# Optimization experiments

Measured on AMD Instinct MI355X. Metric: run time of the kernel, lower is better.

## Reference

```python
import jax, jax.numpy as jnp
import numpy as np

DIM = 2048
NUM_HEADS = 4  # hardcoded in RetNext.__init__
HEAD_DIM = DIM // NUM_HEADS
B, T = 4, 4096


def setup_inputs() -> dict:
    key = jax.random.key(0)
    ks = jax.random.split(key, 7)
    s = 1.0 / np.sqrt(DIM)  # roughly nn.Linear init scale
    return {
        "x": jax.random.normal(ks[0], (B, T, DIM), dtype=jnp.float32),
        "Wk": jax.random.normal(ks[1], (DIM, DIM), dtype=jnp.float32) * s,
        "bk": jax.random.normal(ks[2], (DIM,), dtype=jnp.float32) * s,
        "Wq": jax.random.normal(ks[3], (DIM, DIM), dtype=jnp.float32) * s,
        "bq": jax.random.normal(ks[4], (DIM,), dtype=jnp.float32) * s,
        "Wv": jax.random.normal(ks[5], (DIM, DIM), dtype=jnp.float32) * s,
        "bv": jax.random.normal(ks[6], (DIM,), dtype=jnp.float32) * s,
    }


def reference(x, Wk, bk, Wq, bq, Wv, bv):
    bsz, seq_len, _ = x.shape
    # nn.Linear: y = x @ W.T + b
    k = x @ Wk.T + bk
    q = x @ Wq.T + bq
    v = x @ Wv.T + bv
    # (b, s, h, d) -> (b, h, s, d)
    k = k.reshape(bsz, seq_len, NUM_HEADS, HEAD_DIM).transpose(0, 2, 1, 3)
    q = q.reshape(bsz, seq_len, NUM_HEADS, HEAD_DIM).transpose(0, 2, 1, 3)
    v = v.reshape(bsz, seq_len, NUM_HEADS, HEAD_DIM).transpose(0, 2, 1, 3)
    # states = k^T @ v : (b, h, d, d)
    states = jnp.einsum("bhsd,bhse->bhde", k, v)
    # out = q @ states : (b, h, s, d) -- returned WITHOUT reshape, as in the source
    out = jnp.einsum("bhsd,bhde->bhse", q, states)
    return out
```

## Files before the change

### kernel.cpp

```cpp
#include <hip/hip_runtime.h>
#include <cstdint>
#include <cstddef>

typedef __bf16 bf16;
typedef bf16 bf16x8 __attribute__((ext_vector_type(8)));
typedef float f32x4 __attribute__((ext_vector_type(4)));
typedef unsigned short u16;
typedef u16 u16x4 __attribute__((ext_vector_type(4)));
typedef u16 u16x8 __attribute__((ext_vector_type(8)));

__device__ __forceinline__ u16 f2bf(float f) {
    uint32_t u = __builtin_bit_cast(uint32_t, f);
    u += 0x7FFFu + ((u >> 16) & 1u);
    return (u16)(u >> 16);
}

#define AS1C(p) ((const __attribute__((address_space(1))) uint32_t*)(p))
#define AS3(p)  ((__attribute__((address_space(3))) uint32_t*)(p))
#define MFMA16  __builtin_amdgcn_mfma_f32_16x16x32_bf16

__device__ __forceinline__ void gemm_core(const bf16* __restrict__ Ablk,
                                          const bf16* __restrict__ Btblk,
                                          int lda, int ldb, int K,
                                          f32x4 acc[4][4])
{
    __shared__ bf16 lA[4096];
    __shared__ bf16 lB[4096];

    const int tid  = threadIdx.x;
    const int wave = tid >> 6;
    const int lane = tid & 63;
    const int lrow = lane >> 2;
    const int kcol = (lane & 3) << 3;

    const bf16* ga0 = Ablk  + (size_t)(wave * 32 + lrow) * lda + kcol;
    const bf16* ga1 = ga0 + (size_t)16 * lda;
    const bf16* gb0 = Btblk + (size_t)(wave * 32 + lrow) * ldb + kcol;
    const bf16* gb1 = gb0 + (size_t)16 * ldb;
    bf16* la0 = &lA[wave * 1024];
    bf16* la1 = &lA[wave * 1024 + 512];
    bf16* lb0 = &lB[wave * 1024];
    bf16* lb1 = &lB[wave * 1024 + 512];

    const int wm    = (wave >> 1) * 64;
    const int wn    = (wave & 1) * 64;
    const int col16 = lane & 15;
    const int quad  = lane >> 4;
    const bf16* pa = &lA[(wm + col16) * 32 + quad * 8];
    const bf16* pb = &lB[(wn + col16) * 32 + quad * 8];

    for (int kb = 0; kb < K; kb += 32) {
        __builtin_amdgcn_global_load_lds(AS1C(ga0 + kb), AS3(la0), 16, 0, 0);
        __builtin_amdgcn_global_load_lds(AS1C(ga1 + kb), AS3(la1), 16, 0, 0);
        __builtin_amdgcn_global_load_lds(AS1C(gb0 + kb), AS3(lb0), 16, 0, 0);
        __builtin_amdgcn_global_load_lds(AS1C(gb1 + kb), AS3(lb1), 16, 0, 0);
        __syncthreads();

        bf16x8 av[4], bv[4];
        #pragma unroll
        for (int i = 0; i < 4; ++i) av[i] = *(const bf16x8*)(pa + i * 512);
        #pragma unroll
        for (int i = 0; i < 4; ++i) bv[i] = *(const bf16x8*)(pb + i * 512);

        #pragma unroll
        for (int mi = 0; mi < 4; ++mi)
            #pragma unroll
            for (int ni = 0; ni < 4; ++ni)
                acc[mi][ni] = MFMA16(av[mi], bv[ni], acc[mi][ni], 0, 0, 0);
        __syncthreads();
    }
}

__global__ __launch_bounds__(256) void cast_bf16(const float* __restrict__ src,
                                                 u16* __restrict__ dst, int n8)
{
    int i = blockIdx.x * 256 + threadIdx.x;
    if (i >= n8) return;
    const float4* s = (const float4*)src + (size_t)i * 2;
    float4 f0 = s[0], f1 = s[1];
    u16x8 o;
    o[0] = f2bf(f0.x); o[1] = f2bf(f0.y); o[2] = f2bf(f0.z); o[3] = f2bf(f0.w);
    o[4] = f2bf(f1.x); o[5] = f2bf(f1.y); o[6] = f2bf(f1.z); o[7] = f2bf(f1.w);
    *((u16x8*)dst + i) = o;
}

__global__ __launch_bounds__(512, 2) void gemm_qkv(
    const bf16* __restrict__ xb,
    const bf16* __restrict__ Wkb, const bf16* __restrict__ Wqb, const bf16* __restrict__ Wvb,
    const float* __restrict__ bk, const float* __restrict__ bq, const float* __restrict__ bv,
    u16* __restrict__ qout, u16* __restrict__ kT, u16* __restrict__ vT)
{
    __shared__ bf16 smem[49152];
    char* sm = (char*)smem;

    const int bx = blockIdx.x;
    const int by = blockIdx.y;
    const int region = by >> 3;
    const int nloc = (by & 7) << 8;

    const bf16* W     = (region == 0) ? Wkb : (region == 1) ? Wqb : Wvb;
    const float* bias = (region == 0) ? bk  : (region == 1) ? bq  : bv;

    const bf16* Ablk = xb + (size_t)bx * 256 * 2048;
    const bf16* Bblk = W  + (size_t)nloc * 2048;
    const int lda = 2048, ldb = 2048;
    const int NT = 2048 / 32;

    const int tid  = threadIdx.x;
    const int wave = tid >> 6;
    const int lane = tid & 63;
    const int col16 = lane & 15;
    const int quad  = lane >> 4;
    const int wm = (wave >> 2) * 128;
    const int wn = (wave & 3) * 64;

    const int P0 = tid * 16;
    const int T0 = P0 ^ ((P0 >> 2) & 0x70) ^ ((P0 >> 4) & 0x10);
    const int r0 = T0 >> 6;
    const int ce = (T0 & 63) >> 1;
    const bf16* gA0 = Ablk + (size_t)r0 * lda + ce;
    const bf16* gA1 = Ablk + (size_t)(r0 + 128) * lda + ce;
    const bf16* gB0 = Bblk + (size_t)r0 * ldb + ce;
    const bf16* gB1 = Bblk + (size_t)(r0 + 128) * ldb + ce;
    const int dA0 = wave * 1024;
    const int dA1 = 8192  + wave * 1024;
    const int dB0 = 16384 + wave * 1024;
    const int dB1 = 24576 + wave * 1024;

    int offA[8], offB[4];
    #pragma unroll
    for (int mi = 0; mi < 8; ++mi) {
        int T = (wm + mi * 16 + col16) * 64 + quad * 16;
        offA[mi] = T ^ ((T >> 2) & 0x70);
    }
    #pragma unroll
    for (int ni = 0; ni < 4; ++ni) {
        int T = (wn + ni * 16 + col16) * 64 + quad * 16;
        offB[ni] = 16384 + (T ^ ((T >> 2) & 0x70));
    }

    f32x4 acc[8][4] = {};

#define GLD(src, dst) __builtin_amdgcn_global_load_lds(AS1C(src), AS3(sm + (dst)), 16, 0, 0)

    GLD(gA0,      0 + dA0); GLD(gB0,      0 + dB0);
    GLD(gA1,      0 + dA1); GLD(gB1,      0 + dB1);
    GLD(gA0 + 32, 32768 + dA0); GLD(gB0 + 32, 32768 + dB0);
    GLD(gA1 + 32, 32768 + dA1); GLD(gB1 + 32, 32768 + dB1);
    asm volatile("s_waitcnt vmcnt(4)" ::: "memory");
    __builtin_amdgcn_s_barrier();
    asm volatile("" ::: "memory");

    int buf = 0, sb = 2;
    for (int t = 0; t < NT; ++t) {
        const int  bb  = buf * 32768;
        const int  sbb = sb  * 32768;
        const int  kb  = (t + 2) * 32;
        const bool st  = (t + 2) < NT;

        bf16x8 a0 = *(const bf16x8*)(sm + bb + offA[0]);
        bf16x8 a1 = *(const bf16x8*)(sm + bb + offA[1]);
        bf16x8 a2 = *(const bf16x8*)(sm + bb + offA[2]);
        bf16x8 a3 = *(const bf16x8*)(sm + bb + offA[3]);
        bf16x8 b0 = *(const bf16x8*)(sm + bb + offB[0]);
        bf16x8 b1 = *(const bf16x8*)(sm + bb + offB[1]);
        bf16x8 b2 = *(const bf16x8*)(sm + bb + offB[2]);
        bf16x8 b3 = *(const bf16x8*)(sm + bb + offB[3]);
        if (st) { GLD(gA0 + kb, sbb + dA0); GLD(gB0 + kb, sbb + dB0); }
        __builtin_amdgcn_s_setprio(1);
        acc[0][0] = MFMA16(a0, b0, acc[0][0], 0, 0, 0);
        acc[0][1] = MFMA16(a0, b1, acc[0][1], 0, 0, 0);
        acc[0][2] = MFMA16(a0, b2, acc[0][2], 0, 0, 0);
        acc[0][3] = MFMA16(a0, b3, acc[0][3], 0, 0, 0);
        acc[1][0] = MFMA16(a1, b0, acc[1][0], 0, 0, 0);
        acc[1][1] = MFMA16(a1, b1, acc[1][1], 0, 0, 0);
        acc[1][2] = MFMA16(a1, b2, acc[1][2], 0, 0, 0);
        acc[1][3] = MFMA16(a1, b3, acc[1][3], 0, 0, 0);
        acc[2][0] = MFMA16(a2, b0, acc[2][0], 0, 0, 0);
        acc[2][1] = MFMA16(a2, b1, acc[2][1], 0, 0, 0);
        acc[2][2] = MFMA16(a2, b2, acc[2][2], 0, 0, 0);
        acc[2][3] = MFMA16(a2, b3, acc[2][3], 0, 0, 0);
        acc[3][0] = MFMA16(a3, b0, acc[3][0], 0, 0, 0);
        acc[3][1] = MFMA16(a3, b1, acc[3][1], 0, 0, 0);
        acc[3][2] = MFMA16(a3, b2, acc[3][2], 0, 0, 0);
        acc[3][3] = MFMA16(a3, b3, acc[3][3], 0, 0, 0);
        __builtin_amdgcn_s_setprio(0);
        __builtin_amdgcn_s_barrier();
        asm volatile("" ::: "memory");

        bf16x8 a4 = *(const bf16x8*)(sm + bb + offA[4]);
        bf16x8 a5 = *(const bf16x8*)(sm + bb + offA[5]);
        bf16x8 a6 = *(const bf16x8*)(sm + bb + offA[6]);
        bf16x8 a7 = *(const bf16x8*)(sm + bb + offA[7]);
        if (st) { GLD(gA1 + kb, sbb + dA1); GLD(gB1 + kb, sbb + dB1); }
        if (st) { asm volatile("s_waitcnt vmcnt(4)" ::: "memory"); }
        else    { asm volatile("s_waitcnt vmcnt(0)" ::: "memory"); }
        __builtin_amdgcn_s_setprio(1);
        acc[4][0] = MFMA16(a4, b0, acc[4][0], 0, 0, 0);
        acc[4][1] = MFMA16(a4, b1, acc[4][1], 0, 0, 0);
        acc[4][2] = MFMA16(a4, b2, acc[4][2], 0, 0, 0);
        acc[4][3] = MFMA16(a4, b3, acc[4][3], 0, 0, 0);
        acc[5][0] = MFMA16(a5, b0, acc[5][0], 0, 0, 0);
        acc[5][1] = MFMA16(a5, b1, acc[5][1], 0, 0, 0);
        acc[5][2] = MFMA16(a5, b2, acc[5][2], 0, 0, 0);
        acc[5][3] = MFMA16(a5, b3, acc[5][3], 0, 0, 0);
        acc[6][0] = MFMA16(a6, b0, acc[6][0], 0, 0, 0);
        acc[6][1] = MFMA16(a6, b1, acc[6][1], 0, 0, 0);
        acc[6][2] = MFMA16(a6, b2, acc[6][2], 0, 0, 0);
        acc[6][3] = MFMA16(a6, b3, acc[6][3], 0, 0, 0);
        acc[7][0] = MFMA16(a7, b0, acc[7][0], 0, 0, 0);
        acc[7][1] = MFMA16(a7, b1, acc[7][1], 0, 0, 0);
        acc[7][2] = MFMA16(a7, b2, acc[7][2], 0, 0, 0);
        acc[7][3] = MFMA16(a7, b3, acc[7][3], 0, 0, 0);
        __builtin_amdgcn_s_setprio(0);
        __builtin_amdgcn_s_barrier();
        asm volatile("" ::: "memory");

        buf = (buf == 2) ? 0 : buf + 1;
        sb  = (sb  == 2) ? 0 : sb  + 1;
    }
#undef GLD

    if (region == 1) {
        #pragma unroll
        for (int mi = 0; mi < 8; ++mi) {
            int row = bx * 256 + wm + mi * 16 + quad * 4;
            #pragma unroll
            for (int ni = 0; ni < 4; ++ni) {
                int col = nloc + wn + ni * 16 + col16;
                float b = bias[col];
                #pragma unroll
                for (int r = 0; r < 4; ++r)
                    qout[(size_t)(row + r) * 2048 + col] = f2bf(acc[mi][ni][r] + b);
            }
        }
    } else {
        u16* T = (region == 0) ? kT : vT;
        const int b_ = bx >> 4;
        const int h_ = nloc >> 9;
        const int bh = b_ * 4 + h_;
        #pragma unroll
        for (int mi = 0; mi < 8; ++mi) {
            int s = ((bx & 15) * 256) + wm + mi * 16 + quad * 4;
            #pragma unroll
            for (int ni = 0; ni < 4; ++ni) {
                int fcol = nloc + wn + ni * 16 + col16;
                int d = fcol & 511;
                float b = bias[fcol];
                u16x4 p;
                #pragma unroll
                for (int r = 0; r < 4; ++r) p[r] = f2bf(acc[mi][ni][r] + b);
                *(u16x4*)&T[((size_t)(bh * 512 + d)) * 4096 + s] = p;
            }
        }
    }
}

__global__ __launch_bounds__(256) void gemm_states(
    const u16* __restrict__ vT, const u16* __restrict__ kT, u16* __restrict__ ST)
{
    const int bh = blockIdx.z;
    const int m0 = blockIdx.x * 128;
    const int n0 = blockIdx.y * 128;

    f32x4 acc[4][4] = {};
    gemm_core((const bf16*)vT + (size_t)bh * 2097152 + (size_t)m0 * 4096,
              (const bf16*)kT + (size_t)bh * 2097152 + (size_t)n0 * 4096,
              4096, 4096, 4096, acc);

    const int lane = threadIdx.x & 63, wave = threadIdx.x >> 6;
    const int wm = (wave >> 1) * 64, wn = (wave & 1) * 64;
    const int col16 = lane & 15, quad = lane >> 4;
    #pragma unroll
    for (int mi = 0; mi < 4; ++mi) {
        int row = m0 + wm + mi * 16 + quad * 4;
        #pragma unroll
        for (int ni = 0; ni < 4; ++ni) {
            int col = n0 + wn + ni * 16 + col16;
            #pragma unroll
            for (int r = 0; r < 4; ++r)
                ST[(size_t)bh * 262144 + (size_t)(row + r) * 512 + col] =
                    f2bf(acc[mi][ni][r]);
        }
    }
}

__global__ __launch_bounds__(256) void gemm_out(
    const u16* __restrict__ qb, const u16* __restrict__ ST, float* __restrict__ out)
{
    const int bh = blockIdx.z;
    const int b_ = bh >> 2, h_ = bh & 3;
    const int m0 = blockIdx.x * 128;
    const int n0 = blockIdx.y * 128;

    f32x4 acc[4][4] = {};
    gemm_core((const bf16*)qb + ((size_t)(b_ * 4096 + m0)) * 2048 + h_ * 512,
              (const bf16*)ST + (size_t)bh * 262144 + (size_t)n0 * 512,
              2048, 512, 512, acc);

    const int lane = threadIdx.x & 63, wave = threadIdx.x >> 6;
    const int wm = (wave >> 1) * 64, wn = (wave & 1) * 64;
    const int col16 = lane & 15, quad = lane >> 4;
    #pragma unroll
    for (int mi = 0; mi < 4; ++mi) {
        int row = m0 + wm + mi * 16 + quad * 4;
        #pragma unroll
        for (int ni = 0; ni < 4; ++ni) {
            int col = n0 + wn + ni * 16 + col16;
            #pragma unroll
            for (int r = 0; r < 4; ++r)
                out[(size_t)bh * 2097152 + (size_t)(row + r) * 512 + col] =
                    acc[mi][ni][r];
        }
    }
}

extern "C" void kernel_launch(void* const* d_in, const int* in_sizes, int n_in,
                              void* d_out, int out_size, void* d_ws, size_t ws_size,
                              hipStream_t stream)
{
    (void)in_sizes; (void)n_in; (void)out_size; (void)ws_size;
    const float* x  = (const float*)d_in[0];
    const float* Wk = (const float*)d_in[1];
    const float* bk = (const float*)d_in[2];
    const float* Wq = (const float*)d_in[3];
    const float* bq = (const float*)d_in[4];
    const float* Wv = (const float*)d_in[5];
    const float* bv = (const float*)d_in[6];
    float* out = (float*)d_out;

    u16* ws  = (u16*)d_ws;
    u16* xb  = ws;
    u16* Wkb = ws  + 33554432;
    u16* Wqb = Wkb + 4194304;
    u16* Wvb = Wqb + 4194304;
    u16* qb  = Wvb + 4194304;
    u16* kT  = qb  + 33554432;
    u16* vT  = kT  + 33554432;
    u16* ST  = vT  + 33554432;

    cast_bf16<<<16384, 256, 0, stream>>>(x,  xb,  4194304);
    cast_bf16<<<2048,  256, 0, stream>>>(Wk, Wkb, 524288);
    cast_bf16<<<2048,  256, 0, stream>>>(Wq, Wqb, 524288);
    cast_bf16<<<2048,  256, 0, stream>>>(Wv, Wvb, 524288);

    gemm_qkv<<<dim3(64, 24), 512, 0, stream>>>(
        (const bf16*)xb, (const bf16*)Wkb, (const bf16*)Wqb, (const bf16*)Wvb,
        bk, bq, bv, qb, kT, vT);

    gemm_states<<<dim3(4, 4, 16), 256, 0, stream>>>(vT, kT, ST);

    gemm_out<<<dim3(32, 4, 16), 256, 0, stream>>>(qb, ST, out);
}
```

Before: 818.2 us.

## Split-K the states GEMM into two halves and restructure qkv loop barriers

The states GEMM (K=4096) previously launched only 256 blocks; it now splits K into two halves across 512 blocks, writing fp32 partials into the reused xb workspace. A new reduce_cast kernel sums the partials and converts them to bf16. The aim is to fill more of the GPU's compute units during the states GEMM, at the cost of extra fp32 traffic and one more launch. Separately, the qkv GEMM main loop gains an extra barrier, an lgkmcnt(0) wait and sched_barrier before each MFMA cluster, which pins the LDS-read/MFMA ordering but adds sync points.

```diff
diff --git a/kernel.cpp b/kernel.cpp
--- a/kernel.cpp
+++ b/kernel.cpp
@@ -82,6 +82,19 @@
     o[0] = f2bf(f0.x); o[1] = f2bf(f0.y); o[2] = f2bf(f0.z); o[3] = f2bf(f0.w);
     o[4] = f2bf(f1.x); o[5] = f2bf(f1.y); o[6] = f2bf(f1.z); o[7] = f2bf(f1.w);
     *((u16x8*)dst + i) = o;
+}
+
+__global__ __launch_bounds__(256) void reduce_cast(const float* __restrict__ sp,
+                                                   u16* __restrict__ dst, int n4)
+{
+    int i = blockIdx.x * 256 + threadIdx.x;
+    if (i >= n4) return;
+    float4 a = ((const float4*)sp)[i];
+    float4 b = ((const float4*)(sp + 4194304))[i];
+    u16x4 o;
+    o[0] = f2bf(a.x + b.x); o[1] = f2bf(a.y + b.y);
+    o[2] = f2bf(a.z + b.z); o[3] = f2bf(a.w + b.w);
+    ((u16x4*)dst)[i] = o;
 }
 
 __global__ __launch_bounds__(512, 2) void gemm_qkv(
@@ -167,6 +180,10 @@
         bf16x8 b2 = *(const bf16x8*)(sm + bb + offB[2]);
         bf16x8 b3 = *(const bf16x8*)(sm + bb + offB[3]);
         if (st) { GLD(gA0 + kb, sbb + dA0); GLD(gB0 + kb, sbb + dB0); }
+        asm volatile("" ::: "memory");
+        __builtin_amdgcn_s_barrier();
+        asm volatile("s_waitcnt lgkmcnt(0)" ::: "memory");
+        __builtin_amdgcn_sched_barrier(0);
         __builtin_amdgcn_s_setprio(1);
         acc[0][0] = MFMA16(a0, b0, acc[0][0], 0, 0, 0);
         acc[0][1] = MFMA16(a0, b1, acc[0][1], 0, 0, 0);
@@ -185,6 +202,7 @@
         acc[3][2] = MFMA16(a3, b2, acc[3][2], 0, 0, 0);
         acc[3][3] = MFMA16(a3, b3, acc[3][3], 0, 0, 0);
         __builtin_amdgcn_s_setprio(0);
+        asm volatile("" ::: "memory");
         __builtin_amdgcn_s_barrier();
         asm volatile("" ::: "memory");
 
@@ -195,6 +213,10 @@
         if (st) { GLD(gA1 + kb, sbb + dA1); GLD(gB1 + kb, sbb + dB1); }
         if (st) { asm volatile("s_waitcnt vmcnt(4)" ::: "memory"); }
         else    { asm volatile("s_waitcnt vmcnt(0)" ::: "memory"); }
+        asm volatile("" ::: "memory");
+        __builtin_amdgcn_s_barrier();
+        asm volatile("s_waitcnt lgkmcnt(0)" ::: "memory");
+        __builtin_amdgcn_sched_barrier(0);
         __builtin_amdgcn_s_setprio(1);
         acc[4][0] = MFMA16(a4, b0, acc[4][0], 0, 0, 0);
         acc[4][1] = MFMA16(a4, b1, acc[4][1], 0, 0, 0);
@@ -213,6 +235,7 @@
         acc[7][2] = MFMA16(a7, b2, acc[7][2], 0, 0, 0);
         acc[7][3] = MFMA16(a7, b3, acc[7][3], 0, 0, 0);
         __builtin_amdgcn_s_setprio(0);
+        asm volatile("" ::: "memory");
         __builtin_amdgcn_s_barrier();
         asm volatile("" ::: "memory");
 
@@ -257,17 +280,22 @@
 }
 
 __global__ __launch_bounds__(256) void gemm_states(
-    const u16* __restrict__ vT, const u16* __restrict__ kT, u16* __restrict__ ST)
-{
-    const int bh = blockIdx.z;
+    const u16* __restrict__ vT, const u16* __restrict__ kT, float* __restrict__ SP)
+{
+    const int z  = blockIdx.z;
+    const int bh = z >> 1;
+    const int kh = z & 1;
     const int m0 = blockIdx.x * 128;
     const int n0 = blockIdx.y * 128;
 
     f32x4 acc[4][4] = {};
-    gemm_core((const bf16*)vT + (size_t)bh * 2097152 + (size_t)m0 * 4096,
-              (const bf16*)kT + (size_t)bh * 2097152 + (size_t)n0 * 4096,
-              4096, 4096, 4096, acc);
-
+    const size_t base = (size_t)bh * 2097152;
+    const size_t koff = (size_t)kh * 2048;
+    gemm_core((const bf16*)vT + base + (size_t)m0 * 4096 + koff,
+              (const bf16*)kT + base + (size_t)n0 * 4096 + koff,
+              4096, 4096, 2048, acc);
+
+    float* P = SP + (size_t)kh * 4194304 + (size_t)bh * 262144;
     const int lane = threadIdx.x & 63, wave = threadIdx.x >> 6;
     const int wm = (wave >> 1) * 64, wn = (wave & 1) * 64;
     const int col16 = lane & 15, quad = lane >> 4;
@@ -279,8 +307,7 @@
             int col = n0 + wn + ni * 16 + col16;
             #pragma unroll
             for (int r = 0; r < 4; ++r)
-                ST[(size_t)bh * 262144 + (size_t)(row + r) * 512 + col] =
-                    f2bf(acc[mi][ni][r]);
+                P[(size_t)(row + r) * 512 + col] = acc[mi][ni][r];
         }
     }
 }
@@ -338,6 +365,7 @@
     u16* kT  = qb  + 33554432;
     u16* vT  = kT  + 33554432;
     u16* ST  = vT  + 33554432;
+    float* SP = (float*)xb;
 
     cast_bf16<<<16384, 256, 0, stream>>>(x,  xb,  4194304);
     cast_bf16<<<2048,  256, 0, stream>>>(Wk, Wkb, 524288);
@@ -348,7 +376,8 @@
         (const bf16*)xb, (const bf16*)Wkb, (const bf16*)Wqb, (const bf16*)Wvb,
         bk, bq, bv, qb, kT, vT);
 
-    gemm_states<<<dim3(4, 4, 16), 256, 0, stream>>>(vT, kT, ST);
+    gemm_states<<<dim3(4, 4, 32), 256, 0, stream>>>(vT, kT, SP);
+    reduce_cast<<<4096, 256, 0, stream>>>(SP, ST, 1048576);
 
     gemm_out<<<dim3(32, 4, 16), 256, 0, stream>>>(qb, ST, out);
 }
```

Measured after the change: 828.3 us. No clear change (+1.2%).
